# Kernel tuning notes

Hardware: AMD Instinct MI355X
Metric: run time of the kernel (lower is better)

## Reference

```python
import jax, jax.numpy as jnp
import numpy as np

SPARSITY = 0.5  # cur_sparsity set during training; 0.0 default would make masking a no-op
WEIGHT_BETA = 1.0
MASK_ALPHA1 = 1.0
MASK_ALPHA2 = 1.0


def binarize(mask_scores, sparsity):
    # SparseBinarizer.forward: prune (set to 0) the `num_prune` smallest scores globally.
    num_prune = int(mask_scores.size * sparsity)  # static: sparsity is a Python float
    flat = mask_scores.reshape(-1)
    prune_idx = jnp.argsort(flat)[:num_prune]
    mask = jnp.ones_like(flat).at[prune_idx].set(0.0)
    return mask.reshape(mask_scores.shape)


def setup_inputs() -> dict:
    key = jax.random.key(0)
    ks = jax.random.split(key, 9)
    out_f, in_f, r = 4096, 4096, 8
    tokens = 8192  # batch 4 * seq 2048
    return {
        "x": jax.random.normal(ks[0], (tokens, in_f), dtype=jnp.float32),
        "weight": jax.random.normal(ks[1], (out_f, in_f), dtype=jnp.float32) * 0.02,
        "bias": jax.random.normal(ks[2], (out_f,), dtype=jnp.float32) * 0.02,
        "weight_U": jax.random.normal(ks[3], (out_f, r), dtype=jnp.float32),
        "weight_V": jnp.zeros((r, in_f), dtype=jnp.float32),
        "mask_scores_A": jax.random.normal(ks[4], (out_f, r), dtype=jnp.float32),
        "mask_scores_B": jnp.zeros((r, in_f), dtype=jnp.float32),
        "mask_scores_R": jnp.zeros((out_f,), dtype=jnp.float32),
        "mask_scores_C": jnp.zeros((in_f,), dtype=jnp.float32),
    }


def reference(x, weight, bias, weight_U, weight_V, mask_scores_A, mask_scores_B,
              mask_scores_R, mask_scores_C):
    # weight = W + beta * U @ V   (low-rank weight reconstruction)
    w = weight + WEIGHT_BETA * (weight_U @ weight_V)
    # mask_scores = |w| + a1 * A @ B + a2 * (R[:,None] + C[None,:])
    mask_scores = (jnp.abs(w)
                   + MASK_ALPHA1 * (mask_scores_A @ mask_scores_B)
                   + MASK_ALPHA2 * (mask_scores_R[:, None] + mask_scores_C[None, :]))
    mask = binarize(mask_scores, SPARSITY)
    masked_weight = mask * w  # [out_f, in_f]
    # nn.Linear: x @ W^T + b
    return x @ masked_weight.T + bias
```

## Files before the change

### kernel.cpp

```cpp
#include <hip/hip_runtime.h>
#include <stdint.h>

#define TOKENS 8192
#define OUT_F  4096
#define IN_F   4096
#define RNK    8
#define KPRUNE 8388608u
#define CAP3   16384u

typedef unsigned short u16;
typedef float  f32x4  __attribute__((ext_vector_type(4)));
typedef short  bf16x8 __attribute__((ext_vector_type(8)));
typedef unsigned short u16x4 __attribute__((ext_vector_type(4)));
typedef unsigned short u16x8 __attribute__((ext_vector_type(8)));

#define XB_OFF    0ull
#define WB_OFF    67108864ull
#define KEYS_OFF  100663296ull
#define CTL_OFF   167772160ull
#define H1_OFF    0
#define H2_OFF    16384
#define SEL_OFF   32768
#define CNT3_OFF  32800
#define LIST3_OFF 32804
#define CTL_ZERO_U32 8201

__device__ __forceinline__ u16 f2bf(float f) {
    uint32_t u = __float_as_uint(f);
    u += 0x7fffu + ((u >> 16) & 1u);
    return (u16)(u >> 16);
}

__device__ __forceinline__ uint32_t fkey(float s) {
    uint32_t u = __float_as_uint(s);
    return (u & 0x80000000u) ? ~u : (u | 0x80000000u);
}

__global__ void convx_kernel(const float* __restrict__ x, u16* __restrict__ xB,
                             uint32_t* __restrict__ ctl)
{
    const int t = threadIdx.x;
    if (blockIdx.x < 34) {
        const int i = blockIdx.x * 256 + t;
        if (i < CTL_ZERO_U32) ctl[i] = 0u;
    }
    const size_t idx = (size_t)blockIdx.x * 256 + t;
    const float4* xv = (const float4*)x;
    float4 a = xv[idx*2];
    float4 b = xv[idx*2 + 1];
    u16x8 o;
    o[0]=f2bf(a.x); o[1]=f2bf(a.y); o[2]=f2bf(a.z); o[3]=f2bf(a.w);
    o[4]=f2bf(b.x); o[5]=f2bf(b.y); o[6]=f2bf(b.z); o[7]=f2bf(b.w);
    *((u16x8*)xB + idx) = o;
}

__global__ void prep_kernel(const float* __restrict__ W, const float* __restrict__ U,
                            const float* __restrict__ V, const float* __restrict__ A,
                            const float* __restrict__ B, const float* __restrict__ R,
                            const float* __restrict__ C, u16* __restrict__ wB,
                            uint32_t* __restrict__ keys, uint32_t* __restrict__ hist1)
{
    __shared__ uint32_t lh[4096];
    const int o0 = blockIdx.x * 2, t = threadIdx.x;
    for (int b = t; b < 4096; b += 256) lh[b] = 0u;
    float uu0[RNK], uu1[RNK], aa0[RNK], aa1[RNK];
#pragma unroll
    for (int r = 0; r < RNK; ++r) {
        uu0[r] = U[o0*RNK + r];       uu1[r] = U[(o0+1)*RNK + r];
        aa0[r] = A[o0*RNK + r];       aa1[r] = A[(o0+1)*RNK + r];
    }
    const float ro0 = R[o0], ro1 = R[o0 + 1];
    __syncthreads();
    for (int j = 0; j < IN_F/1024; ++j) {
        const int i = j*1024 + t*4;
        const float4 cc = *(const float4*)&C[i];
        float4 w0 = *(const float4*)&W[(size_t)o0*IN_F + i];
        float4 w1 = *(const float4*)&W[(size_t)(o0+1)*IN_F + i];
#pragma unroll
        for (int r = 0; r < RNK; ++r) {
            const float4 v4 = *(const float4*)&V[r*IN_F + i];
            const float a0 = uu0[r], a1 = uu1[r];
            w0.x = fmaf(a0, v4.x, w0.x); w0.y = fmaf(a0, v4.y, w0.y);
            w0.z = fmaf(a0, v4.z, w0.z); w0.w = fmaf(a0, v4.w, w0.w);
            w1.x = fmaf(a1, v4.x, w1.x); w1.y = fmaf(a1, v4.y, w1.y);
            w1.z = fmaf(a1, v4.z, w1.z); w1.w = fmaf(a1, v4.w, w1.w);
        }
        float4 s0, s1;
        s0.x = fabsf(w0.x); s0.y = fabsf(w0.y); s0.z = fabsf(w0.z); s0.w = fabsf(w0.w);
        s1.x = fabsf(w1.x); s1.y = fabsf(w1.y); s1.z = fabsf(w1.z); s1.w = fabsf(w1.w);
#pragma unroll
        for (int r = 0; r < RNK; ++r) {
            const float4 b4 = *(const float4*)&B[r*IN_F + i];
            const float a0 = aa0[r], a1 = aa1[r];
            s0.x = fmaf(a0, b4.x, s0.x); s0.y = fmaf(a0, b4.y, s0.y);
            s0.z = fmaf(a0, b4.z, s0.z); s0.w = fmaf(a0, b4.w, s0.w);
            s1.x = fmaf(a1, b4.x, s1.x); s1.y = fmaf(a1, b4.y, s1.y);
            s1.z = fmaf(a1, b4.z, s1.z); s1.w = fmaf(a1, b4.w, s1.w);
        }
        s0.x += ro0 + cc.x; s0.y += ro0 + cc.y; s0.z += ro0 + cc.z; s0.w += ro0 + cc.w;
        s1.x += ro1 + cc.x; s1.y += ro1 + cc.y; s1.z += ro1 + cc.z; s1.w += ro1 + cc.w;
        uint4 k0, k1;
        k0.x = fkey(s0.x); k0.y = fkey(s0.y); k0.z = fkey(s0.z); k0.w = fkey(s0.w);
        k1.x = fkey(s1.x); k1.y = fkey(s1.y); k1.z = fkey(s1.z); k1.w = fkey(s1.w);
        *(uint4*)&keys[(size_t)o0*IN_F + i]     = k0;
        *(uint4*)&keys[(size_t)(o0+1)*IN_F + i] = k1;
        u16x4 b0, b1;
        b0[0]=f2bf(w0.x); b0[1]=f2bf(w0.y); b0[2]=f2bf(w0.z); b0[3]=f2bf(w0.w);
        b1[0]=f2bf(w1.x); b1[1]=f2bf(w1.y); b1[2]=f2bf(w1.z); b1[3]=f2bf(w1.w);
        *(u16x4*)&wB[(size_t)o0*IN_F + i]     = b0;
        *(u16x4*)&wB[(size_t)(o0+1)*IN_F + i] = b1;
        atomicAdd(&lh[k0.x >> 20], 1u); atomicAdd(&lh[k0.y >> 20], 1u);
        atomicAdd(&lh[k0.z >> 20], 1u); atomicAdd(&lh[k0.w >> 20], 1u);
        atomicAdd(&lh[k1.x >> 20], 1u); atomicAdd(&lh[k1.y >> 20], 1u);
        atomicAdd(&lh[k1.z >> 20], 1u); atomicAdd(&lh[k1.w >> 20], 1u);
    }
    __syncthreads();
    for (int b = t; b < 4096; b += 256) { uint32_t c = lh[b]; if (c) atomicAdd(&hist1[b], c); }
}

__global__ void select_kernel(const uint32_t* __restrict__ hist, uint32_t* sel, int mode)
{
    __shared__ uint32_t lh[4096];
    __shared__ uint32_t part[256];
    __shared__ uint32_t sseg[2];
    const int t = threadIdx.x;
    const uint32_t c1v = sel[1];
    const uint32_t k = (mode == 0) ? KPRUNE : (KPRUNE - c1v);
    for (int b = t; b < 4096; b += 256) lh[b] = hist[b];
    __syncthreads();
    uint32_t s = 0;
    for (int j = 0; j < 16; ++j) s += lh[t*16 + j];
    part[t] = s;
    __syncthreads();
    uint32_t pre = 0;
    for (int tt = 0; tt < t; ++tt) pre += part[tt];
    if (pre < k && pre + part[t] >= k) { sseg[0] = (uint32_t)t; sseg[1] = pre; }
    __syncthreads();
    const int seg = (int)sseg[0];
    const uint32_t accb = sseg[1];
    if (t < 16) {
        uint32_t pre2 = 0;
        for (int j = 0; j < t; ++j) pre2 += lh[seg*16 + j];
        const uint32_t c = lh[seg*16 + t];
        const uint32_t below = accb + pre2;
        if (below < k && below + c >= k) {
            const uint32_t bin = (uint32_t)(seg*16 + t);
            if (mode == 0) { sel[0] = bin; sel[1] = below; }
            else           { sel[2] = bin; sel[3] = c1v + below; }
        }
    }
}

__global__ void hist2_kernel(const uint32_t* __restrict__ keys, const uint32_t* __restrict__ sel,
                             uint32_t* __restrict__ hist2)
{
    __shared__ uint32_t lh[4096];
    const int o = blockIdx.x, t = threadIdx.x;
    const uint32_t b1 = sel[0];
    for (int b = t; b < 4096; b += 256) lh[b] = 0u;
    __syncthreads();
    const uint32_t* kp = keys + (size_t)o*IN_F + t*16;
#pragma unroll
    for (int q = 0; q < 4; ++q) {
        uint4 kv = *(const uint4*)(kp + q*4);
        if ((kv.x >> 20) == b1) atomicAdd(&lh[(kv.x >> 8) & 0xFFFu], 1u);
        if ((kv.y >> 20) == b1) atomicAdd(&lh[(kv.y >> 8) & 0xFFFu], 1u);
        if ((kv.z >> 20) == b1) atomicAdd(&lh[(kv.z >> 8) & 0xFFFu], 1u);
        if ((kv.w >> 20) == b1) atomicAdd(&lh[(kv.w >> 8) & 0xFFFu], 1u);
    }
    __syncthreads();
    for (int b = t; b < 4096; b += 256) { uint32_t c = lh[b]; if (c) atomicAdd(&hist2[b], c); }
}

__global__ void apply_kernel(const uint32_t* __restrict__ keys, const uint32_t* __restrict__ sel,
                             u16* __restrict__ wB, uint32_t* __restrict__ cnt3,
                             uint32_t* __restrict__ list3)
{
    const uint32_t pfx = (sel[0] << 12) | sel[2];
    const size_t base = ((size_t)blockIdx.x * 256 + threadIdx.x) * 16;
    uint32_t kv[16];
#pragma unroll
    for (int q = 0; q < 4; ++q) *(uint4*)(kv + q*4) = *(const uint4*)(keys + base + q*4);
    uint4 wraw[2];
    wraw[0] = *(const uint4*)(wB + base);
    wraw[1] = *(const uint4*)(wB + base + 8);
    u16* wv = (u16*)wraw;
#pragma unroll
    for (int e = 0; e < 16; ++e) {
        const uint32_t hi = kv[e] >> 8;
        if (hi < pfx) wv[e] = 0u;
        else if (hi == pfx) {
            uint32_t s = atomicAdd(cnt3, 1u);
            if (s < CAP3) list3[s] = ((uint32_t)(base + e) << 8) | (kv[e] & 0xFFu);
        }
    }
    *(uint4*)(wB + base)     = wraw[0];
    *(uint4*)(wB + base + 8) = wraw[1];
}

__global__ void selfix_kernel(const uint32_t* __restrict__ sel, const uint32_t* __restrict__ cnt3,
                              const uint32_t* __restrict__ list3, u16* __restrict__ wB)
{
    __shared__ uint32_t lst[CAP3];
    __shared__ uint32_t hist[256];
    __shared__ uint32_t sv[2];
    const int t = threadIdx.x;
    uint32_t n = *cnt3; if (n > CAP3) n = CAP3;
    hist[t] = 0u;
    __syncthreads();
    for (uint32_t i = t; i < n; i += 256) {
        const uint32_t e = list3[i];
        lst[i] = e;
        atomicAdd(&hist[e & 0xFFu], 1u);
    }
    __syncthreads();
    const uint32_t k3 = KPRUNE - sel[3];
    uint32_t pre = 0;
    for (int b = 0; b < t; ++b) pre += hist[b];
    if (pre < k3 && pre + hist[t] >= k3) {
        sv[0] = (uint32_t)t;
        sv[1] = k3 - pre;
    }
    __syncthreads();
    const uint32_t b3 = sv[0], p = sv[1];
    for (uint32_t i = t; i < n; i += 256) {
        const uint32_t e = lst[i];
        const uint32_t lo = e & 0xFFu;
        if (lo < b3) { wB[e >> 8] = 0u; continue; }
        if (lo != b3) continue;
        uint32_t rank = 0;
        for (uint32_t j = 0; j < n; ++j) {
            const uint32_t f = lst[j];
            rank += ((f & 0xFFu) == b3 && f < e) ? 1u : 0u;
        }
        if (rank < p) wB[e >> 8] = 0u;
    }
}

#define A0H0   0
#define A0H1_0 16384
#define A0H1_1 32768
#define B0S    49152
#define A1H0   81920
#define A1H1_0 98304
#define A1H1_1 114688
#define B1S    131072

__device__ __forceinline__ void gl_lds16(const char* src, char* dst) {
    __builtin_amdgcn_global_load_lds((const __attribute__((address_space(1))) void*)src,
                                     (__attribute__((address_space(3))) void*)dst, 16, 0, 0);
}

__global__ __launch_bounds__(512, 2) void gemm256_kernel(const u16* __restrict__ xB,
                                                         const u16* __restrict__ wB,
                                                         const float* __restrict__ bias,
                                                         float* __restrict__ out)
{
    __shared__ char ldsc[163840];
    const int t    = threadIdx.x;
    const int lane = t & 63;
    const int wid  = t >> 6;
    const int wm   = wid >> 2;
    const int wn   = wid & 3;
    const int bid  = blockIdx.x;
    const int bn   = bid & 15;
    const int bm   = bid >> 4;

    const int l15 = lane & 15;
    const int kb  = (lane >> 4) << 4;
    const int sw  = (lane & 7) << 4;
    const int bAo = (16*wm + l15) * 128 + kb;
    const int bB  = (64*wn + l15) * 128 + kb;

    const int scol = ((t & 7) * 16) ^ (((t >> 3) & 7) << 4);
    const char* pA = (const char*)xB + ((size_t)(bm*256 + (t >> 3))) * (IN_F*2) + scol;
    const char* pB = (const char*)wB + ((size_t)(bn*256 + (t >> 3))) * (IN_F*2) + scol;
    const int tb16 = t * 16;

#define STAGEH(pG, slot, h, tile) do {                                        \
    const char* _s = (pG) + (size_t)(tile)*128 + (size_t)(h)*(128*IN_F*2);    \
    char* _d = ldsc + (slot) + tb16;                                          \
    gl_lds16(_s, _d);                                                         \
    gl_lds16(_s + (size_t)(64*IN_F*2), _d + 8192);                            \
} while (0)

    f32x4  acc[8][4] = {};
    bf16x8 b[4][2];
    bf16x8 a[2][2];

#define LOADB(reg) do {                                                       \
    _Pragma("unroll") for (int ni = 0; ni < 4; ++ni)                          \
    _Pragma("unroll") for (int kk = 0; kk < 2; ++kk)                          \
        b[ni][kk] = *(const bf16x8*)(ldsc + (reg) +                           \
                      ((bB + ni*2048 + kk*64) ^ sw));                         \
} while (0)

#define LOADA(slot, q, mo) do {                                               \
    _Pragma("unroll") for (int mm = 0; mm < 2; ++mm)                          \
    _Pragma("unroll") for (int kk = 0; kk < 2; ++kk)                          \
        a[mm][kk] = *(const bf16x8*)(ldsc + (slot) +                          \
                      (((2*(q)+mm-(mo))*4096 + bAo + kk*64) ^ sw));           \
} while (0)

#define MFMAQ(q) do {                                                         \
    _Pragma("unroll") for (int mm = 0; mm < 2; ++mm)                          \
    _Pragma("unroll") for (int ni = 0; ni < 4; ++ni)                          \
    _Pragma("unroll") for (int kk = 0; kk < 2; ++kk)                          \
        acc[2*(q)+mm][ni] = __builtin_amdgcn_mfma_f32_16x16x32_bf16(          \
            a[mm][kk], b[ni][kk], acc[2*(q)+mm][ni], 0, 0, 0);                \
} while (0)

#define PH_TAIL(q)                                                            \
    __builtin_amdgcn_s_barrier();                                             \
    asm volatile("s_waitcnt lgkmcnt(0)" ::: "memory");                        \
    __builtin_amdgcn_s_setprio(1);                                            \
    MFMAQ(q);                                                                 \
    __builtin_amdgcn_s_setprio(0);                                            \
    __builtin_amdgcn_s_barrier();

#define STQ(q) do {                                                           \
    _Pragma("unroll") for (int mm = 0; mm < 2; ++mm) {                        \
        const int r0 = orow0 + 32*(2*(q)+mm);                                 \
        _Pragma("unroll") for (int ni = 0; ni < 4; ++ni) {                    \
            f32x4 v = acc[2*(q)+mm][ni];                                      \
            const int col = ocol0 + ni*16;                                    \
            _Pragma("unroll") for (int e = 0; e < 4; ++e)                     \
                out[(size_t)(r0 + e)*OUT_F + col] = v[e] + bv[ni];            \
        }                                                                     \
    }                                                                         \
} while (0)

#define PH_TAIL_ST(q)                                                         \
    __builtin_amdgcn_s_barrier();                                             \
    asm volatile("s_waitcnt lgkmcnt(0)" ::: "memory");                        \
    __builtin_amdgcn_s_setprio(1);                                            \
    MFMAQ(q);                                                                 \
    __builtin_amdgcn_s_setprio(0);                                            \
    STQ(q);                                                                   \
    __builtin_amdgcn_s_barrier();

    STAGEH(pA, A0H1_0, 1, 0);
    STAGEH(pB, B0S,         0, 0);
    STAGEH(pB, B0S + 16384, 1, 0);
    STAGEH(pA, A0H0, 0, 0);
    STAGEH(pA, A1H1_0, 1, 1);
    STAGEH(pB, B1S,         0, 1);
    STAGEH(pB, B1S + 16384, 1, 1);
    STAGEH(pA, A1H0, 0, 1);
    asm volatile("s_waitcnt vmcnt(8)" ::: "memory");
    __builtin_amdgcn_s_barrier();

#pragma unroll 1
    for (int j = 0; j < 31; ++j) {
        const int se = 2*j + 2;
        const int so = 2*j + 3;
        const int pc = j & 1;
        const int a0h1c = pc ? A0H1_1 : A0H1_0;
        const int a0h1n = pc ? A0H1_0 : A0H1_1;
        const int a1h1c = pc ? A1H1_1 : A1H1_0;
        const int a1h1n = pc ? A1H1_0 : A1H1_1;

        LOADB(B0S); LOADA(A0H0, 0, 0);
        STAGEH(pA, a0h1n, 1, se);
        asm volatile("s_waitcnt lgkmcnt(8)" ::: "memory");
        PH_TAIL(0)
        LOADA(A0H0, 1, 0);
        STAGEH(pB, B0S, 0, se);
        PH_TAIL(1)
        LOADA(a0h1c, 2, 4);
        STAGEH(pB, B0S + 16384, 1, se);
        PH_TAIL(2)
        LOADA(a0h1c, 3, 4);
        STAGEH(pA, A0H0, 0, se);
        asm volatile("s_waitcnt vmcnt(8)" ::: "memory");
        PH_TAIL(3)

        LOADB(B1S); LOADA(A1H0, 0, 0);
        STAGEH(pA, a1h1n, 1, so);
        asm volatile("s_waitcnt lgkmcnt(8)" ::: "memory");
        PH_TAIL(0)
        LOADA(A1H0, 1, 0);
        STAGEH(pB, B1S, 0, so);
        PH_TAIL(1)
        LOADA(a1h1c, 2, 4);
        STAGEH(pB, B1S + 16384, 1, so);
        PH_TAIL(2)
        LOADA(a1h1c, 3, 4);
        STAGEH(pA, A1H0, 0, so);
        asm volatile("s_waitcnt vmcnt(8)" ::: "memory");
        PH_TAIL(3)
    }

    const int orow0 = bm*256 + 16*wm + ((lane >> 4) << 2);
    const int ocol0 = bn*256 + 64*wn + l15;
    float bv[4];
#pragma unroll
    for (int ni = 0; ni < 4; ++ni) bv[ni] = bias[ocol0 + ni*16];

    LOADB(B0S); LOADA(A0H0, 0, 0);
    asm volatile("s_waitcnt lgkmcnt(8)" ::: "memory");
    PH_TAIL(0)
    LOADA(A0H0, 1, 0);
    PH_TAIL(1)
    LOADA(A0H1_1, 2, 4);
    PH_TAIL(2)
    LOADA(A0H1_1, 3, 4);
    PH_TAIL(3)

    asm volatile("s_waitcnt vmcnt(0)" ::: "memory");
    __builtin_amdgcn_s_barrier();
    LOADB(B1S); LOADA(A1H0, 0, 0);
    asm volatile("s_waitcnt lgkmcnt(8)" ::: "memory");
    PH_TAIL_ST(0)
    LOADA(A1H0, 1, 0);
    PH_TAIL_ST(1)
    LOADA(A1H1_1, 2, 4);
    PH_TAIL_ST(2)
    LOADA(A1H1_1, 3, 4);
    PH_TAIL_ST(3)

#undef STAGEH
#undef LOADB
#undef LOADA
#undef MFMAQ
#undef PH_TAIL
#undef PH_TAIL_ST
#undef STQ
}

extern "C" void kernel_launch(void* const* d_in, const int* in_sizes, int n_in,
                              void* d_out, int out_size, void* d_ws, size_t ws_size,
                              hipStream_t stream)
{
    const float* x    = (const float*)d_in[0];
    const float* W    = (const float*)d_in[1];
    const float* bias = (const float*)d_in[2];
    const float* U    = (const float*)d_in[3];
    const float* V    = (const float*)d_in[4];
    const float* A    = (const float*)d_in[5];
    const float* B    = (const float*)d_in[6];
    const float* R    = (const float*)d_in[7];
    const float* C    = (const float*)d_in[8];
    float* out = (float*)d_out;

    char* ws = (char*)d_ws;
    u16*      xB    = (u16*)(ws + XB_OFF);
    u16*      wB    = (u16*)(ws + WB_OFF);
    uint32_t* keys  = (uint32_t*)(ws + KEYS_OFF);
    uint32_t* ctl   = (uint32_t*)(ws + CTL_OFF);
    uint32_t* h1    = (uint32_t*)((char*)ctl + H1_OFF);
    uint32_t* h2    = (uint32_t*)((char*)ctl + H2_OFF);
    uint32_t* sel   = (uint32_t*)((char*)ctl + SEL_OFF);
    uint32_t* cnt3  = (uint32_t*)((char*)ctl + CNT3_OFF);
    uint32_t* list3 = (uint32_t*)((char*)ctl + LIST3_OFF);

    convx_kernel<<<TOKENS*IN_F/8/256, 256, 0, stream>>>(x, xB, ctl);
    prep_kernel<<<OUT_F/2, 256, 0, stream>>>(W, U, V, A, B, R, C, wB, keys, h1);
    select_kernel<<<1, 256, 0, stream>>>(h1, sel, 0);
    hist2_kernel<<<OUT_F, 256, 0, stream>>>(keys, sel, h2);
    select_kernel<<<1, 256, 0, stream>>>(h2, sel, 1);
    apply_kernel<<<OUT_F, 256, 0, stream>>>(keys, sel, wB, cnt3, list3);
    selfix_kernel<<<1, 256, 0, stream>>>(sel, cnt3, list3, wB);
    gemm256_kernel<<<(TOKENS/256)*(OUT_F/256), 512, 0, stream>>>(xB, wB, bias, out);
}
```

Before: 401.6 us.

## Restructure GEMM LDS tile layout to 64-byte half-K rows with precomputed pointers

Changes the shared-memory layout of the A and B tiles. Each 128-byte K-slice is now split into two 64-byte halves stored 8 KB apart, with a different XOR swizzle based on row bits. Global-to-LDS staging loads now cover 4 threads per row instead of 8. Fragment reads use precomputed base pointers with constant offsets, which removes per-load XOR address math and aims for conflict-free ds_reads. This risks bank conflicts or mismatched indexing if the new swizzle does not line up with the staging pattern.

```diff
diff --git a/kernel.cpp b/kernel.cpp
--- a/kernel.cpp
+++ b/kernel.cpp
@@ -268,38 +268,42 @@
 
     const int l15 = lane & 15;
     const int kb  = (lane >> 4) << 4;
-    const int sw  = (lane & 7) << 4;
-    const int bAo = (16*wm + l15) * 128 + kb;
-    const int bB  = (64*wn + l15) * 128 + kb;
-
-    const int scol = ((t & 7) * 16) ^ (((t >> 3) & 7) << 4);
-    const char* pA = (const char*)xB + ((size_t)(bm*256 + (t >> 3))) * (IN_F*2) + scol;
-    const char* pB = (const char*)wB + ((size_t)(bn*256 + (t >> 3))) * (IN_F*2) + scol;
+    const int rowA = 16*wm + l15;
+    const int rowB = (wn & 1)*64 + l15;
+    const int baseA = rowA*64 + (kb ^ (((rowA >> 1) & 3) << 4));
+    const int baseB = rowB*64 + (kb ^ (((rowB >> 1) & 3) << 4));
+    const char* aB0 = ldsc + baseA;
+    const char* aB1 = ldsc + A1H0 + baseA;
+    const char* bB0 = ldsc + B0S + (wn >> 1)*16384 + baseB;
+    const char* bB1 = bB0 + (B1S - B0S);
+
+    const int scol = ((t & 3) * 16) ^ (((t >> 3) & 3) << 4);
+    const char* pA = (const char*)xB + ((size_t)(bm*256 + (t >> 2))) * (IN_F*2) + scol;
+    const char* pB = (const char*)wB + ((size_t)(bn*256 + (t >> 2))) * (IN_F*2) + scol;
     const int tb16 = t * 16;
 
 #define STAGEH(pG, slot, h, tile) do {                                        \
     const char* _s = (pG) + (size_t)(tile)*128 + (size_t)(h)*(128*IN_F*2);    \
     char* _d = ldsc + (slot) + tb16;                                          \
     gl_lds16(_s, _d);                                                         \
-    gl_lds16(_s + (size_t)(64*IN_F*2), _d + 8192);                            \
+    gl_lds16(_s + 64, _d + 8192);                                             \
 } while (0)
 
     f32x4  acc[8][4] = {};
     bf16x8 b[4][2];
     bf16x8 a[2][2];
 
-#define LOADB(reg) do {                                                       \
+#define LOADB(bp) do {                                                        \
     _Pragma("unroll") for (int ni = 0; ni < 4; ++ni)                          \
     _Pragma("unroll") for (int kk = 0; kk < 2; ++kk)                          \
-        b[ni][kk] = *(const bf16x8*)(ldsc + (reg) +                           \
-                      ((bB + ni*2048 + kk*64) ^ sw));                         \
+        b[ni][kk] = *(const bf16x8*)((bp) + ni*1024 + kk*8192);               \
 } while (0)
 
-#define LOADA(slot, q, mo) do {                                               \
+#define LOADA(ap, slot, q, mo) do {                                           \
     _Pragma("unroll") for (int mm = 0; mm < 2; ++mm)                          \
     _Pragma("unroll") for (int kk = 0; kk < 2; ++kk)                          \
-        a[mm][kk] = *(const bf16x8*)(ldsc + (slot) +                          \
-                      (((2*(q)+mm-(mo))*4096 + bAo + kk*64) ^ sw));           \
+        a[mm][kk] = *(const bf16x8*)((ap) + (slot) +                          \
+                      (2*(q)+mm-(mo))*2048 + kk*8192);                        \
 } while (0)
 
 #define MFMAQ(q) do {                                                         \
@@ -360,32 +364,32 @@
         const int a1h1c = pc ? A1H1_1 : A1H1_0;
         const int a1h1n = pc ? A1H1_0 : A1H1_1;
 
-        LOADB(B0S); LOADA(A0H0, 0, 0);
+        LOADB(bB0); LOADA(aB0, A0H0, 0, 0);
         STAGEH(pA, a0h1n, 1, se);
         asm volatile("s_waitcnt lgkmcnt(8)" ::: "memory");
         PH_TAIL(0)
-        LOADA(A0H0, 1, 0);
+        LOADA(aB0, A0H0, 1, 0);
         STAGEH(pB, B0S, 0, se);
         PH_TAIL(1)
-        LOADA(a0h1c, 2, 4);
+        LOADA(aB0, a0h1c, 2, 4);
         STAGEH(pB, B0S + 16384, 1, se);
         PH_TAIL(2)
-        LOADA(a0h1c, 3, 4);
+        LOADA(aB0, a0h1c, 3, 4);
         STAGEH(pA, A0H0, 0, se);
         asm volatile("s_waitcnt vmcnt(8)" ::: "memory");
         PH_TAIL(3)
 
-        LOADB(B1S); LOADA(A1H0, 0, 0);
+        LOADB(bB1); LOADA(aB1, 0, 0, 0);
         STAGEH(pA, a1h1n, 1, so);
         asm volatile("s_waitcnt lgkmcnt(8)" ::: "memory");
         PH_TAIL(0)
-        LOADA(A1H0, 1, 0);
+        LOADA(aB1, 0, 1, 0);
         STAGEH(pB, B1S, 0, so);
         PH_TAIL(1)
-        LOADA(a1h1c, 2, 4);
+        LOADA(aB1, a1h1c - A1H0, 2, 4);
         STAGEH(pB, B1S + 16384, 1, so);
         PH_TAIL(2)
-        LOADA(a1h1c, 3, 4);
+        LOADA(aB1, a1h1c - A1H0, 3, 4);
         STAGEH(pA, A1H0, 0, so);
         asm volatile("s_waitcnt vmcnt(8)" ::: "memory");
         PH_TAIL(3)
@@ -397,26 +401,26 @@
 #pragma unroll
     for (int ni = 0; ni < 4; ++ni) bv[ni] = bias[ocol0 + ni*16];
 
-    LOADB(B0S); LOADA(A0H0, 0, 0);
+    LOADB(bB0); LOADA(aB0, A0H0, 0, 0);
     asm volatile("s_waitcnt lgkmcnt(8)" ::: "memory");
     PH_TAIL(0)
-    LOADA(A0H0, 1, 0);
+    LOADA(aB0, A0H0, 1, 0);
     PH_TAIL(1)
-    LOADA(A0H1_1, 2, 4);
+    LOADA(aB0, A0H1_1, 2, 4);
     PH_TAIL(2)
-    LOADA(A0H1_1, 3, 4);
+    LOADA(aB0, A0H1_1, 3, 4);
     PH_TAIL(3)
 
     asm volatile("s_waitcnt vmcnt(0)" ::: "memory");
     __builtin_amdgcn_s_barrier();
-    LOADB(B1S); LOADA(A1H0, 0, 0);
+    LOADB(bB1); LOADA(aB1, 0, 0, 0);
     asm volatile("s_waitcnt lgkmcnt(8)" ::: "memory");
     PH_TAIL_ST(0)
-    LOADA(A1H0, 1, 0);
+    LOADA(aB1, 0, 1, 0);
     PH_TAIL_ST(1)
-    LOADA(A1H1_1, 2, 4);
+    LOADA(aB1, A1H1_1 - A1H0, 2, 4);
     PH_TAIL_ST(2)
-    LOADA(A1H1_1, 3, 4);
+    LOADA(aB1, A1H1_1 - A1H0, 3, 4);
     PH_TAIL_ST(3)
 
 #undef STAGEH
```

Result: no change. 400.4 us (-0.3%).
